# Kernel tuning notes

Measured on AMD Instinct MI355X. Metric: run time of the kernel, lower is better.

## Reference

```python
import jax, jax.numpy as jnp
import numpy as np

NUM_EXPERTS = 4096
NUM_KEYS = 64  # floor(sqrt(num_experts))
TOP_K = 16
NORM_TOPK = False
BN_EPS = 1e-5


def setup_inputs() -> dict:
    key = jax.random.key(0)
    ks = jax.random.split(key, 7)
    B, S, H, I = 2, 2048, 2048, 8192
    s = 0.02
    return {
        "hidden_states": jax.random.normal(ks[0], (B, S, H), jnp.float32),
        "router_gate_w": jax.random.normal(ks[1], (2 * NUM_KEYS, H), jnp.float32) * s,
        "down_embed": jax.random.normal(ks[2], (NUM_EXPERTS, H), jnp.float32) * s,
        "up_embed": jax.random.normal(ks[3], (NUM_EXPERTS, H), jnp.float32) * s,
        "gate_w": jax.random.normal(ks[4], (I, H), jnp.float32) * s,
        "up_w": jax.random.normal(ks[5], (I, H), jnp.float32) * s,
        "down_w": jax.random.normal(ks[6], (H, I), jnp.float32) * s,
    }


def reference(hidden_states, router_gate_w, down_embed, up_embed, gate_w, up_w, down_w):
    B, S, H = hidden_states.shape
    x = hidden_states.reshape(-1, H)  # [N, H]

    # BatchNorm1d(affine=False), training-mode batch statistics (biased var)
    mu = jnp.mean(x, axis=0, keepdims=True)
    var = jnp.mean(jnp.square(x - mu), axis=0, keepdims=True)
    xn = (x - mu) * jax.lax.rsqrt(var + BN_EPS)

    # product-key router: logits [2, N, num_keys]
    rlog = (xn @ router_gate_w.T).reshape(-1, 2, NUM_KEYS).transpose(1, 0, 2)
    logp = jax.nn.log_softmax(rlog, axis=-1)

    # full product scores [N, nk, nk]; top-k over nk*nk candidates
    full = logp[0][:, :, None] + logp[1][:, None, :]
    scores, indices = jax.lax.top_k(full.reshape(-1, NUM_KEYS * NUM_KEYS), TOP_K)
    routing_weights = jnp.exp(scores)  # [N, k]
    if NORM_TOPK:
        routing_weights = routing_weights / jnp.sum(routing_weights, axis=-1, keepdims=True)

    # PEER-style expert: scalar key match then weighted up-embedding sum
    d = down_embed[indices]  # [N, k, H]
    u = up_embed[indices]    # [N, k, H]
    h = jnp.einsum('nh,nkh->nk', x, d)
    experts_states = jnp.einsum('nk,nk,nkh->nh', routing_weights, h, u)

    # dense gated MLP (silu)
    mlp = (jax.nn.silu(x @ gate_w.T) * (x @ up_w.T)) @ down_w.T

    out = (mlp + experts_states).reshape(B, S, H)
    return out, rlog
```

## Files before the change

kernel.cpp:

```cpp
#include <hip/hip_runtime.h>
#include <stdint.h>

#define H_DIM 2048
#define N_TOK 4096
#define I_DIM 8192

typedef __attribute__((ext_vector_type(8))) short short8;
typedef __attribute__((ext_vector_type(4))) float f32x4;

typedef const __attribute__((address_space(1))) unsigned int* gp_t;
typedef __attribute__((address_space(3))) unsigned int* lp_t;

__device__ __forceinline__ void gload16(const unsigned short* g, short* l) {
    __builtin_amdgcn_global_load_lds((gp_t)g, (lp_t)l, 16, 0, 0);
}

__device__ __forceinline__ unsigned short f2bf(float f) {
    union { float f; unsigned int u; } c; c.f = f;
    unsigned int u = c.u;
    return (unsigned short)((u + 0x7FFFu + ((u >> 16) & 1u)) >> 16);
}
__device__ __forceinline__ float bf2f(unsigned short u) {
    union { unsigned int i; float f; } c; c.i = ((unsigned int)u) << 16;
    return c.f;
}

__device__ __forceinline__ float wmax64(float v) {
#pragma unroll
    for (int o = 32; o > 0; o >>= 1) v = fmaxf(v, __shfl_xor(v, o));
    return v;
}
__device__ __forceinline__ float wsum64(float v) {
#pragma unroll
    for (int o = 32; o > 0; o >>= 1) v += __shfl_xor(v, o);
    return v;
}

template<int K, int RSTEP, int LSTEP>
__device__ __forceinline__ void stage4(const unsigned short* src, short* dst) {
#pragma unroll
    for (int j = 0; j < 4; ++j)
        gload16(src + (size_t)j * RSTEP * K, dst + j * LSTEP);
}
template<int K, int RSTEP, int LSTEP>
__device__ __forceinline__ void stage2(const unsigned short* src, short* dst) {
#pragma unroll
    for (int j = 0; j < 2; ++j)
        gload16(src + (size_t)j * RSTEP * K, dst + j * LSTEP);
}

__global__ __launch_bounds__(256) void bn_stats(const float* __restrict__ x,
                                                float* __restrict__ ps, float* __restrict__ pq) {
    int col = blockIdx.x * 256 + threadIdx.x;
    int r0  = blockIdx.y * 128;
    float s = 0.f, q = 0.f;
    for (int r = 0; r < 128; ++r) {
        float v = x[(size_t)(r0 + r) * H_DIM + col];
        s += v; q += v * v;
    }
    ps[blockIdx.y * H_DIM + col] = s;
    pq[blockIdx.y * H_DIM + col] = q;
}

__global__ __launch_bounds__(256) void bn_finalize(const float* __restrict__ ps, const float* __restrict__ pq,
                                                   float* __restrict__ mu, float* __restrict__ rsig) {
    int c = blockIdx.x * 256 + threadIdx.x;
    float s = 0.f, q = 0.f;
    for (int i = 0; i < 32; ++i) { s += ps[i * H_DIM + c]; q += pq[i * H_DIM + c]; }
    float m = s * (1.f / N_TOK);
    float v = q * (1.f / N_TOK) - m * m;
    mu[c] = m;
    rsig[c] = rsqrtf(v + 1e-5f);
}

__global__ __launch_bounds__(256) void cvt_all(const float* __restrict__ gw, const float* __restrict__ uw,
                                               const float* __restrict__ dw, const float* __restrict__ de,
                                               const float* __restrict__ ue, const float* __restrict__ x,
                                               unsigned short* __restrict__ gwb, unsigned short* __restrict__ uwb,
                                               unsigned short* __restrict__ dwb, unsigned short* __restrict__ deb,
                                               unsigned short* __restrict__ ueb, unsigned short* __restrict__ xb) {
    int b = blockIdx.x;
    const float* src; unsigned short* dst; size_t base;
    if      (b < 8192)  { src = gw; dst = gwb; base = (size_t)b; }
    else if (b < 16384) { src = uw; dst = uwb; base = (size_t)(b - 8192); }
    else if (b < 24576) { src = dw; dst = dwb; base = (size_t)(b - 16384); }
    else if (b < 28672) { src = de; dst = deb; base = (size_t)(b - 24576); }
    else if (b < 32768) { src = ue; dst = ueb; base = (size_t)(b - 28672); }
    else                { src = x;  dst = xb;  base = (size_t)(b - 32768); }
    size_t off = (base * 256 + threadIdx.x) * 8;
    float4 a = *(const float4*)(src + off);
    float4 c = *(const float4*)(src + off + 4);
    short8 s;
    s[0]=(short)f2bf(a.x); s[1]=(short)f2bf(a.y); s[2]=(short)f2bf(a.z); s[3]=(short)f2bf(a.w);
    s[4]=(short)f2bf(c.x); s[5]=(short)f2bf(c.y); s[6]=(short)f2bf(c.z); s[7]=(short)f2bf(c.w);
    *(short8*)(dst + off) = s;
}

__global__ __launch_bounds__(256) void cvt_x(const float* __restrict__ x, unsigned short* __restrict__ xb) {
    size_t i = ((size_t)blockIdx.x * 256 + threadIdx.x) * 4;
    float4 v = *(const float4*)(x + i);
    uint2 o;
    o.x = (unsigned)f2bf(v.x) | ((unsigned)f2bf(v.y) << 16);
    o.y = (unsigned)f2bf(v.z) | ((unsigned)f2bf(v.w) << 16);
    *(uint2*)(xb + i) = o;
}

__global__ __launch_bounds__(256) void cvt_w(const float* __restrict__ src, unsigned short* __restrict__ dst) {
    size_t off = ((size_t)blockIdx.x * 256 + threadIdx.x) * 8;
    float4 a = *(const float4*)(src + off);
    float4 b = *(const float4*)(src + off + 4);
    short8 s;
    s[0]=(short)f2bf(a.x); s[1]=(short)f2bf(a.y); s[2]=(short)f2bf(a.z); s[3]=(short)f2bf(a.w);
    s[4]=(short)f2bf(b.x); s[5]=(short)f2bf(b.y); s[6]=(short)f2bf(b.z); s[7]=(short)f2bf(b.w);
    *(short8*)(dst + off) = s;
}

__global__ __launch_bounds__(256) void router_kernel(const float* __restrict__ x, const float* __restrict__ rgw,
                                                     const float* __restrict__ mu, const float* __restrict__ rsig,
                                                     float* __restrict__ rlog) {
    __shared__ float xs[16][65];
    __shared__ float rs[128][65];
    const int t = threadIdx.x;
    const int n0 = blockIdx.x * 16;
    const int tk = t >> 5;
    const int jj = t & 31;
    float acc[2][4] = {{0.f,0.f,0.f,0.f},{0.f,0.f,0.f,0.f}};

    for (int kc = 0; kc < H_DIM; kc += 64) {
        {
            int row = t >> 4, c4 = (t & 15) * 4;
            float4 v = *(const float4*)(x + (size_t)(n0 + row) * H_DIM + kc + c4);
            float4 m = *(const float4*)(mu + kc + c4);
            float4 r = *(const float4*)(rsig + kc + c4);
            xs[row][c4 + 0] = (v.x - m.x) * r.x;
            xs[row][c4 + 1] = (v.y - m.y) * r.y;
            xs[row][c4 + 2] = (v.z - m.z) * r.z;
            xs[row][c4 + 3] = (v.w - m.w) * r.w;
        }
        {
            int row = t >> 1, base = (t & 1) * 32;
            const float* src = rgw + (size_t)row * H_DIM + kc + base;
#pragma unroll
            for (int i = 0; i < 8; ++i) {
                float4 v = *(const float4*)(src + i * 4);
                rs[row][base + i*4 + 0] = v.x;
                rs[row][base + i*4 + 1] = v.y;
                rs[row][base + i*4 + 2] = v.z;
                rs[row][base + i*4 + 3] = v.w;
            }
        }
        __syncthreads();
#pragma unroll 4
        for (int k = 0; k < 64; ++k) {
            float x0 = xs[tk][k], x1 = xs[tk + 8][k];
            float r0 = rs[jj][k], r1 = rs[jj + 32][k], r2 = rs[jj + 64][k], r3 = rs[jj + 96][k];
            acc[0][0] += x0 * r0; acc[0][1] += x0 * r1; acc[0][2] += x0 * r2; acc[0][3] += x0 * r3;
            acc[1][0] += x1 * r0; acc[1][1] += x1 * r1; acc[1][2] += x1 * r2; acc[1][3] += x1 * r3;
        }
        __syncthreads();
    }
#pragma unroll
    for (int a = 0; a < 2; ++a)
#pragma unroll
        for (int b = 0; b < 4; ++b) {
            int n = n0 + tk + 8 * a;
            int j = jj + 32 * b;
            rlog[(size_t)(j >> 6) * (N_TOK * 64) + (size_t)n * 64 + (j & 63)] = acc[a][b];
        }
}

__global__ __launch_bounds__(256) void topk_kernel(const float* __restrict__ rlog,
                                                   float* __restrict__ topw, int* __restrict__ topi) {
    const int lane = threadIdx.x & 63;
    const int n = blockIdx.x * 4 + (threadIdx.x >> 6);

    float a = rlog[(size_t)n * 64 + lane];
    float b = rlog[(size_t)(N_TOK * 64) + (size_t)n * 64 + lane];
    float ma = wmax64(a);
    float lpa = a - ma - logf(wsum64(expf(a - ma)));
    float mb = wmax64(b);
    float lpb = b - mb - logf(wsum64(expf(b - mb)));

    float va = lpa, vb = lpb;
    float tva = -1e30f, tvb = -1e30f; int tia = 0, tib = 0;
    for (int it = 0; it < 16; ++it) {
        float mx = wmax64(va);
        int w = __ffsll(__ballot(va == mx)) - 1;
        if (lane == it) { tva = mx; tia = w; }
        if (lane == w) va = -1e30f;
        mx = wmax64(vb);
        w = __ffsll(__ballot(vb == mx)) - 1;
        if (lane == it) { tvb = mx; tib = w; }
        if (lane == w) vb = -1e30f;
    }
    float av = __shfl(tva, lane >> 2);
    int   ai = __shfl(tia, lane >> 2);
    int   q0 = (lane & 3) * 4;
    float c0 = av + __shfl(tvb, q0 + 0); int b0 = __shfl(tib, q0 + 0);
    float c1 = av + __shfl(tvb, q0 + 1); int b1 = __shfl(tib, q0 + 1);
    float c2 = av + __shfl(tvb, q0 + 2); int b2 = __shfl(tib, q0 + 2);
    float c3 = av + __shfl(tvb, q0 + 3); int b3 = __shfl(tib, q0 + 3);

    for (int it = 0; it < 16; ++it) {
        float lv = c0; int lq = 0;
        if (c1 > lv) { lv = c1; lq = 1; }
        if (c2 > lv) { lv = c2; lq = 2; }
        if (c3 > lv) { lv = c3; lq = 3; }
        float mx = wmax64(lv);
        int w = __ffsll(__ballot(lv == mx)) - 1;
        if (lane == w) {
            int bj;
            switch (lq) {
                case 0:  bj = b0; c0 = -1e30f; break;
                case 1:  bj = b1; c1 = -1e30f; break;
                case 2:  bj = b2; c2 = -1e30f; break;
                default: bj = b3; c3 = -1e30f; break;
            }
            topw[n * 16 + it] = expf(mx);
            topi[n * 16 + it] = ai * 64 + bj;
        }
    }
}

__global__ __launch_bounds__(256) void experts_kernel_b(const float* __restrict__ x, const unsigned short* __restrict__ de,
                                                        const unsigned short* __restrict__ ue, const float* __restrict__ topw,
                                                        const int* __restrict__ topi, float* __restrict__ out) {
    __shared__ float psum[16][4];
    const int n = blockIdx.x;
    const int t = threadIdx.x, lane = t & 63, wid = t >> 6;

    float xr[8];
    {
        float4 v0 = *(const float4*)(x + (size_t)n * H_DIM + t * 8);
        float4 v1 = *(const float4*)(x + (size_t)n * H_DIM + t * 8 + 4);
        xr[0]=v0.x; xr[1]=v0.y; xr[2]=v0.z; xr[3]=v0.w;
        xr[4]=v1.x; xr[5]=v1.y; xr[6]=v1.z; xr[7]=v1.w;
    }
    int   eidx[16];
    float ew[16];
#pragma unroll
    for (int k = 0; k < 16; ++k) { eidx[k] = topi[n * 16 + k]; ew[k] = topw[n * 16 + k]; }

#pragma unroll
    for (int k = 0; k < 16; ++k) {
        short8 d = *(const short8*)(de + (size_t)eidx[k] * H_DIM + t * 8);
        float p = 0.f;
#pragma unroll
        for (int j = 0; j < 8; ++j) p += bf2f((unsigned short)d[j]) * xr[j];
        p = wsum64(p);
        if (lane == 0) psum[k][wid] = p;
    }
    __syncthreads();

    float acc[8] = {0,0,0,0,0,0,0,0};
#pragma unroll
    for (int k = 0; k < 16; ++k) {
        float h = psum[k][0] + psum[k][1] + psum[k][2] + psum[k][3];
        float coef = ew[k] * h;
        short8 u = *(const short8*)(ue + (size_t)eidx[k] * H_DIM + t * 8);
#pragma unroll
        for (int j = 0; j < 8; ++j) acc[j] += coef * bf2f((unsigned short)u[j]);
    }
    float4 o0 = {acc[0], acc[1], acc[2], acc[3]};
    float4 o1 = {acc[4], acc[5], acc[6], acc[7]};
    *(float4*)(out + (size_t)n * H_DIM + t * 8)     = o0;
    *(float4*)(out + (size_t)n * H_DIM + t * 8 + 4) = o1;
}

__global__ __launch_bounds__(256) void experts_kernel(const float* __restrict__ x, const float* __restrict__ de,
                                                      const float* __restrict__ ue, const float* __restrict__ topw,
                                                      const int* __restrict__ topi, float* __restrict__ out) {
    __shared__ float psum[16][4];
    const int n = blockIdx.x;
    const int t = threadIdx.x, lane = t & 63, wid = t >> 6;

    float xr[8];
    {
        float4 v0 = *(const float4*)(x + (size_t)n * H_DIM + t * 8);
        float4 v1 = *(const float4*)(x + (size_t)n * H_DIM + t * 8 + 4);
        xr[0]=v0.x; xr[1]=v0.y; xr[2]=v0.z; xr[3]=v0.w;
        xr[4]=v1.x; xr[5]=v1.y; xr[6]=v1.z; xr[7]=v1.w;
    }
    int   eidx[16];
    float ew[16];
#pragma unroll
    for (int k = 0; k < 16; ++k) { eidx[k] = topi[n * 16 + k]; ew[k] = topw[n * 16 + k]; }

#pragma unroll
    for (int k = 0; k < 16; ++k) {
        const float* dr = de + (size_t)eidx[k] * H_DIM + t * 8;
        float4 v0 = *(const float4*)dr;
        float4 v1 = *(const float4*)(dr + 4);
        float p = v0.x*xr[0] + v0.y*xr[1] + v0.z*xr[2] + v0.w*xr[3]
                + v1.x*xr[4] + v1.y*xr[5] + v1.z*xr[6] + v1.w*xr[7];
        p = wsum64(p);
        if (lane == 0) psum[k][wid] = p;
    }
    __syncthreads();

    float acc[8] = {0,0,0,0,0,0,0,0};
#pragma unroll
    for (int k = 0; k < 16; ++k) {
        float h = psum[k][0] + psum[k][1] + psum[k][2] + psum[k][3];
        float coef = ew[k] * h;
        const float* ur = ue + (size_t)eidx[k] * H_DIM + t * 8;
        float4 v0 = *(const float4*)ur;
        float4 v1 = *(const float4*)(ur + 4);
        acc[0] += coef * v0.x; acc[1] += coef * v0.y; acc[2] += coef * v0.z; acc[3] += coef * v0.w;
        acc[4] += coef * v1.x; acc[5] += coef * v1.y; acc[6] += coef * v1.z; acc[7] += coef * v1.w;
    }
    float4 o0 = {acc[0], acc[1], acc[2], acc[3]};
    float4 o1 = {acc[4], acc[5], acc[6], acc[7]};
    *(float4*)(out + (size_t)n * H_DIM + t * 8)     = o0;
    *(float4*)(out + (size_t)n * H_DIM + t * 8 + 4) = o1;
}

#define SWZB(row, byteoff) ((byteoff) ^ (((row) & 7) << 4))

#define NTGU (H_DIM / 64)

__global__ __launch_bounds__(512, 2) void gemm_gu256(const unsigned short* __restrict__ xb,
                                                     const unsigned short* __restrict__ gwb,
                                                     const unsigned short* __restrict__ uwb,
                                                     unsigned short* __restrict__ act) {
    __shared__ __attribute__((aligned(16))) short sA[2][16384];
    __shared__ __attribute__((aligned(16))) short sBg[2][8192];
    __shared__ __attribute__((aligned(16))) short sBu[2][8192];
    const int t = threadIdx.x;
    const int lane = t & 63, wid = t >> 6;
    const int wm = wid >> 1, wn = wid & 1;
    const int l15 = lane & 15, l4 = lane >> 4;
    const int bid = blockIdx.x;
    const int sw = (bid & 7) * 128 + (bid >> 3);
    const int bx = sw & 63, by = sw >> 6;
    const int row0 = by * 256, col0 = bx * 128;

    const int rseg = lane >> 3;
    const int chunk = (lane & 7) ^ rseg;
    const unsigned short* aSrc = xb  + (size_t)(row0 + wid * 8 + rseg) * H_DIM + chunk * 8;
    const unsigned short* gSrc = gwb + (size_t)(col0 + wid * 8 + rseg) * H_DIM + chunk * 8;
    const unsigned short* uSrc = uwb + (size_t)(col0 + wid * 8 + rseg) * H_DIM + chunk * 8;

    const int swzb = (l15 & 7) << 4;
    const int kx0 = (l4 * 16) ^ swzb;
    const int kx1 = (64 + l4 * 16) ^ swzb;
    const int arow = (wm * 64 + l15) * 64;
    const int brow = (wn * 64 + l15) * 64;

    f32x4 zero = {0.f, 0.f, 0.f, 0.f};
    f32x4 accg[4][4], accu[4][4];
#pragma unroll
    for (int m = 0; m < 4; ++m)
#pragma unroll
        for (int n = 0; n < 4; ++n) { accg[m][n] = zero; accu[m][n] = zero; }

    stage4<H_DIM, 64, 4096>(aSrc, &sA[0][wid * 512]);
    stage2<H_DIM, 64, 4096>(gSrc, &sBg[0][wid * 512]);
    stage2<H_DIM, 64, 4096>(uSrc, &sBu[0][wid * 512]);
    __syncthreads();

    int cur = 0;
    for (int g = 0; g < NTGU; ++g) {
        if (g + 1 < NTGU) {
            stage4<H_DIM, 64, 4096>(aSrc + (size_t)(g + 1) * 64, &sA[cur ^ 1][wid * 512]);
            stage2<H_DIM, 64, 4096>(gSrc + (size_t)(g + 1) * 64, &sBg[cur ^ 1][wid * 512]);
            stage2<H_DIM, 64, 4096>(uSrc + (size_t)(g + 1) * 64, &sBu[cur ^ 1][wid * 512]);
        }
        const short* Ac = &sA[cur][0];
        const short* Gc = &sBg[cur][0];
        const short* Uc = &sBu[cur][0];
        {
            short8 a0[4], bg0[4], bu0[4];
#pragma unroll
            for (int m = 0; m < 4; ++m) a0[m]  = *(const short8*)(Ac + arow + m * 1024 + (kx0 >> 1));
#pragma unroll
            for (int n = 0; n < 4; ++n) bg0[n] = *(const short8*)(Gc + brow + n * 1024 + (kx0 >> 1));
#pragma unroll
            for (int n = 0; n < 4; ++n) bu0[n] = *(const short8*)(Uc + brow + n * 1024 + (kx0 >> 1));
            __builtin_amdgcn_s_setprio(1);
#pragma unroll
            for (int m = 0; m < 4; ++m)
#pragma unroll
                for (int n = 0; n < 4; ++n) {
                    accg[m][n] = __builtin_amdgcn_mfma_f32_16x16x32_bf16(a0[m], bg0[n], accg[m][n], 0, 0, 0);
                    accu[m][n] = __builtin_amdgcn_mfma_f32_16x16x32_bf16(a0[m], bu0[n], accu[m][n], 0, 0, 0);
                }
            __builtin_amdgcn_s_setprio(0);
        }
        {
            short8 a1[4], bg1[4], bu1[4];
#pragma unroll
            for (int m = 0; m < 4; ++m) a1[m]  = *(const short8*)(Ac + arow + m * 1024 + (kx1 >> 1));
#pragma unroll
            for (int n = 0; n < 4; ++n) bg1[n] = *(const short8*)(Gc + brow + n * 1024 + (kx1 >> 1));
#pragma unroll
            for (int n = 0; n < 4; ++n) bu1[n] = *(const short8*)(Uc + brow + n * 1024 + (kx1 >> 1));
            __builtin_amdgcn_s_setprio(1);
#pragma unroll
            for (int m = 0; m < 4; ++m)
#pragma unroll
                for (int n = 0; n < 4; ++n) {
                    accg[m][n] = __builtin_amdgcn_mfma_f32_16x16x32_bf16(a1[m], bg1[n], accg[m][n], 0, 0, 0);
                    accu[m][n] = __builtin_amdgcn_mfma_f32_16x16x32_bf16(a1[m], bu1[n], accu[m][n], 0, 0, 0);
                }
            __builtin_amdgcn_s_setprio(0);
        }
        __syncthreads();
        cur ^= 1;
    }

    const int rbase = row0 + wm * 64, cbase = col0 + wn * 64;
#pragma unroll
    for (int m = 0; m < 4; ++m)
#pragma unroll
        for (int n = 0; n < 4; ++n)
#pragma unroll
            for (int j = 0; j < 4; ++j) {
                int r = rbase + m * 16 + l4 * 4 + j;
                int c2 = cbase + n * 16 + l15;
                float gv = accg[m][n][j];
                float uv = accu[m][n][j];
                float sv = gv / (1.f + expf(-gv));
                act[(size_t)r * I_DIM + c2] = f2bf(sv * uv);
            }
}

#define NTD (I_DIM / 64)

__global__ __launch_bounds__(256, 2) void gemm_down128(const unsigned short* __restrict__ act,
                                                       const unsigned short* __restrict__ dwb,
                                                       float* __restrict__ out) {
    __shared__ __attribute__((aligned(16))) short sA[2][8192];
    __shared__ __attribute__((aligned(16))) short sB[2][8192];
    const int t = threadIdx.x;
    const int lane = t & 63, wid = t >> 6;
    const int wm = wid >> 1, wn = wid & 1;
    const int l15 = lane & 15, l4 = lane >> 4;
    const int bid = blockIdx.x;
    const int sw = (bid & 7) * 64 + (bid >> 3);
    const int bx = sw & 15, by = sw >> 4;
    const int row0 = by * 128, col0 = bx * 128;

    const int rseg = lane >> 3;
    const int chunk = (lane & 7) ^ rseg;
    const unsigned short* aSrc = act + (size_t)(row0 + wid * 8 + rseg) * I_DIM + chunk * 8;
    const unsigned short* bSrc = dwb + (size_t)(col0 + wid * 8 + rseg) * I_DIM + chunk * 8;

    const int swzb = (l15 & 7) << 4;
    const int kx0 = (l4 * 16) ^ swzb;
    const int kx1 = (64 + l4 * 16) ^ swzb;
    const int arow = (wm * 64 + l15) * 64;
    const int brow = (wn * 64 + l15) * 64;

    f32x4 zero = {0.f, 0.f, 0.f, 0.f};
    f32x4 acc[4][4];
#pragma unroll
    for (int m = 0; m < 4; ++m)
#pragma unroll
        for (int n = 0; n < 4; ++n) acc[m][n] = zero;

    stage4<I_DIM, 32, 2048>(aSrc, &sA[0][wid * 512]);
    stage4<I_DIM, 32, 2048>(bSrc, &sB[0][wid * 512]);
    __syncthreads();

    int cur = 0;
    for (int g = 0; g < NTD; ++g) {
        if (g + 1 < NTD) {
            stage4<I_DIM, 32, 2048>(aSrc + (size_t)(g + 1) * 64, &sA[cur ^ 1][wid * 512]);
            stage4<I_DIM, 32, 2048>(bSrc + (size_t)(g + 1) * 64, &sB[cur ^ 1][wid * 512]);
        }
        const short* Ac = &sA[cur][0];
        const short* Bc = &sB[cur][0];
        {
            short8 a0[4], b0[4];
#pragma unroll
            for (int m = 0; m < 4; ++m) a0[m] = *(const short8*)(Ac + arow + m * 1024 + (kx0 >> 1));
#pragma unroll
            for (int n = 0; n < 4; ++n) b0[n] = *(const short8*)(Bc + brow + n * 1024 + (kx0 >> 1));
            __builtin_amdgcn_s_setprio(1);
#pragma unroll
            for (int m = 0; m < 4; ++m)
#pragma unroll
                for (int n = 0; n < 4; ++n)
                    acc[m][n] = __builtin_amdgcn_mfma_f32_16x16x32_bf16(a0[m], b0[n], acc[m][n], 0, 0, 0);
            __builtin_amdgcn_s_setprio(0);
        }
        {
            short8 a1[4], b1[4];
#pragma unroll
            for (int m = 0; m < 4; ++m) a1[m] = *(const short8*)(Ac + arow + m * 1024 + (kx1 >> 1));
#pragma unroll
            for (int n = 0; n < 4; ++n) b1[n] = *(const short8*)(Bc + brow + n * 1024 + (kx1 >> 1));
            __builtin_amdgcn_s_setprio(1);
#pragma unroll
            for (int m = 0; m < 4; ++m)
#pragma unroll
                for (int n = 0; n < 4; ++n)
                    acc[m][n] = __builtin_amdgcn_mfma_f32_16x16x32_bf16(a1[m], b1[n], acc[m][n], 0, 0, 0);
            __builtin_amdgcn_s_setprio(0);
        }
        __syncthreads();
        cur ^= 1;
    }

    const int rbase = row0 + wm * 64, cbase = col0 + wn * 64;
#pragma unroll
    for (int m = 0; m < 4; ++m)
#pragma unroll
        for (int n = 0; n < 4; ++n)
#pragma unroll
            for (int j = 0; j < 4; ++j) {
                int r = rbase + m * 16 + l4 * 4 + j;
                int c2 = cbase + n * 16 + l15;
                out[(size_t)r * H_DIM + c2] += acc[m][n][j];
            }
}

__global__ __launch_bounds__(256) void gemm_gu(const unsigned short* __restrict__ xb,
                                               const float* __restrict__ gw, const float* __restrict__ uw,
                                               unsigned short* __restrict__ act) {
    __shared__ __attribute__((aligned(16))) short As[128 * 64];
    __shared__ __attribute__((aligned(16))) short Bg[128 * 64];
    __shared__ __attribute__((aligned(16))) short Bu[128 * 64];
    const int t = threadIdx.x;
    const int lane = t & 63, wid = t >> 6;
    const int wr = wid >> 1, wc = wid & 1;
    const int l15 = lane & 15, l4 = lane >> 4;
    const int row0 = blockIdx.y * 128;
    const int col0 = blockIdx.x * 128;
    const int srow = t >> 1, shalf = (t & 1) * 32;

    f32x4 zero = {0.f, 0.f, 0.f, 0.f};
    f32x4 accg[4][4], accu[4][4];
#pragma unroll
    for (int m = 0; m < 4; ++m)
#pragma unroll
        for (int n = 0; n < 4; ++n) { accg[m][n] = zero; accu[m][n] = zero; }

    for (int kt = 0; kt < H_DIM; kt += 64) {
        {
            const unsigned short* src = xb + (size_t)(row0 + srow) * H_DIM + kt + shalf;
#pragma unroll
            for (int i = 0; i < 4; ++i) {
                int boff = SWZB(srow, (shalf + i * 8) * 2);
                *(short8*)(As + srow * 64 + (boff >> 1)) = *(const short8*)(src + i * 8);
            }
        }
        {
            const float* g = gw + (size_t)(col0 + srow) * H_DIM + kt + shalf;
            const float* u = uw + (size_t)(col0 + srow) * H_DIM + kt + shalf;
#pragma unroll
            for (int i = 0; i < 4; ++i) {
                int boff = SWZB(srow, (shalf + i * 8) * 2);
                float4 a0 = *(const float4*)(g + i * 8);
                float4 a1 = *(const float4*)(g + i * 8 + 4);
                short8 s;
                s[0]=(short)f2bf(a0.x); s[1]=(short)f2bf(a0.y); s[2]=(short)f2bf(a0.z); s[3]=(short)f2bf(a0.w);
                s[4]=(short)f2bf(a1.x); s[5]=(short)f2bf(a1.y); s[6]=(short)f2bf(a1.z); s[7]=(short)f2bf(a1.w);
                *(short8*)(Bg + srow * 64 + (boff >> 1)) = s;
                float4 b0 = *(const float4*)(u + i * 8);
                float4 b1 = *(const float4*)(u + i * 8 + 4);
                short8 r;
                r[0]=(short)f2bf(b0.x); r[1]=(short)f2bf(b0.y); r[2]=(short)f2bf(b0.z); r[3]=(short)f2bf(b0.w);
                r[4]=(short)f2bf(b1.x); r[5]=(short)f2bf(b1.y); r[6]=(short)f2bf(b1.z); r[7]=(short)f2bf(b1.w);
                *(short8*)(Bu + srow * 64 + (boff >> 1)) = r;
            }
        }
        __syncthreads();
#pragma unroll
        for (int kk = 0; kk < 64; kk += 32) {
            short8 af[4], bgf[4], buf_[4];
#pragma unroll
            for (int m = 0; m < 4; ++m) {
                int row = wr * 64 + m * 16 + l15;
                af[m] = *(const short8*)(As + row * 64 + (SWZB(row, (kk + l4 * 8) * 2) >> 1));
            }
#pragma unroll
            for (int n = 0; n < 4; ++n) {
                int row = wc * 64 + n * 16 + l15;
                int off = row * 64 + (SWZB(row, (kk + l4 * 8) * 2) >> 1);
                bgf[n]  = *(const short8*)(Bg + off);
                buf_[n] = *(const short8*)(Bu + off);
            }
#pragma unroll
            for (int m = 0; m < 4; ++m)
#pragma unroll
                for (int n = 0; n < 4; ++n) {
                    accg[m][n] = __builtin_amdgcn_mfma_f32_16x16x32_bf16(af[m], bgf[n],  accg[m][n], 0, 0, 0);
                    accu[m][n] = __builtin_amdgcn_mfma_f32_16x16x32_bf16(af[m], buf_[n], accu[m][n], 0, 0, 0);
                }
        }
        __syncthreads();
    }
    const int rbase = row0 + wr * 64, cbase = col0 + wc * 64;
#pragma unroll
    for (int m = 0; m < 4; ++m)
#pragma unroll
        for (int n = 0; n < 4; ++n)
#pragma unroll
            for (int j = 0; j < 4; ++j) {
                int r = rbase + m * 16 + l4 * 4 + j;
                int c = cbase + n * 16 + l15;
                float gv = accg[m][n][j];
                float uv = accu[m][n][j];
                float sv = gv / (1.f + expf(-gv));
                act[(size_t)r * I_DIM + c] = f2bf(sv * uv);
            }
}

__global__ __launch_bounds__(256) void gemm_down(const unsigned short* __restrict__ act,
                                                 const float* __restrict__ dw, float* __restrict__ out) {
    __shared__ __attribute__((aligned(16))) short As[128 * 64];
    __shared__ __attribute__((aligned(16))) short Bs[128 * 64];
    const int t = threadIdx.x;
    const int lane = t & 63, wid = t >> 6;
    const int wr = wid >> 1, wc = wid & 1;
    const int l15 = lane & 15, l4 = lane >> 4;
    const int row0 = blockIdx.y * 128;
    const int col0 = blockIdx.x * 128;
    const int srow = t >> 1, shalf = (t & 1) * 32;

    f32x4 zero = {0.f, 0.f, 0.f, 0.f};
    f32x4 acc[4][4];
#pragma unroll
    for (int m = 0; m < 4; ++m)
#pragma unroll
        for (int n = 0; n < 4; ++n) acc[m][n] = zero;

    for (int kt = 0; kt < I_DIM; kt += 64) {
        {
            const unsigned short* src = act + (size_t)(row0 + srow) * I_DIM + kt + shalf;
#pragma unroll
            for (int i = 0; i < 4; ++i) {
                int boff = SWZB(srow, (shalf + i * 8) * 2);
                *(short8*)(As + srow * 64 + (boff >> 1)) = *(const short8*)(src + i * 8);
            }
        }
        {
            const float* g = dw + (size_t)(col0 + srow) * I_DIM + kt + shalf;
#pragma unroll
            for (int i = 0; i < 4; ++i) {
                int boff = SWZB(srow, (shalf + i * 8) * 2);
                float4 a0 = *(const float4*)(g + i * 8);
                float4 a1 = *(const float4*)(g + i * 8 + 4);
                short8 s;
                s[0]=(short)f2bf(a0.x); s[1]=(short)f2bf(a0.y); s[2]=(short)f2bf(a0.z); s[3]=(short)f2bf(a0.w);
                s[4]=(short)f2bf(a1.x); s[5]=(short)f2bf(a1.y); s[6]=(short)f2bf(a1.z); s[7]=(short)f2bf(a1.w);
                *(short8*)(Bs + srow * 64 + (boff >> 1)) = s;
            }
        }
        __syncthreads();
#pragma unroll
        for (int kk = 0; kk < 64; kk += 32) {
            short8 af[4], bf[4];
#pragma unroll
            for (int m = 0; m < 4; ++m) {
                int row = wr * 64 + m * 16 + l15;
                af[m] = *(const short8*)(As + row * 64 + (SWZB(row, (kk + l4 * 8) * 2) >> 1));
            }
#pragma unroll
            for (int n = 0; n < 4; ++n) {
                int row = wc * 64 + n * 16 + l15;
                bf[n] = *(const short8*)(Bs + row * 64 + (SWZB(row, (kk + l4 * 8) * 2) >> 1));
            }
#pragma unroll
            for (int m = 0; m < 4; ++m)
#pragma unroll
                for (int n = 0; n < 4; ++n)
                    acc[m][n] = __builtin_amdgcn_mfma_f32_16x16x32_bf16(af[m], bf[n], acc[m][n], 0, 0, 0);
        }
        __syncthreads();
    }
    const int rbase = row0 + wr * 64, cbase = col0 + wc * 64;
#pragma unroll
    for (int m = 0; m < 4; ++m)
#pragma unroll
        for (int n = 0; n < 4; ++n)
#pragma unroll
            for (int j = 0; j < 4; ++j) {
                int r = rbase + m * 16 + l4 * 4 + j;
                int c = cbase + n * 16 + l15;
                out[(size_t)r * H_DIM + c] += acc[m][n][j];
            }
}

extern "C" void kernel_launch(void* const* d_in, const int* in_sizes, int n_in,
                              void* d_out, int out_size, void* d_ws, size_t ws_size,
                              hipStream_t stream) {
    const float* x   = (const float*)d_in[0];
    const float* rgw = (const float*)d_in[1];
    const float* de  = (const float*)d_in[2];
    const float* ue  = (const float*)d_in[3];
    const float* gw  = (const float*)d_in[4];
    const float* uw  = (const float*)d_in[5];
    const float* dw  = (const float*)d_in[6];
    float* out = (float*)d_out;
    char* ws = (char*)d_ws;

    float* ps   = (float*)(ws + 0);
    float* pq   = (float*)(ws + 262144);
    float* mu   = (float*)(ws + 524288);
    float* rsig = (float*)(ws + 532480);
    float* topw = (float*)(ws + 540672);
    int*   topi = (int*)  (ws + 802816);
    unsigned short* xb  = (unsigned short*)(ws + 1179648);
    unsigned short* act = (unsigned short*)(ws + 17956864);
    unsigned short* gwb = (unsigned short*)(ws + 85065728);
    unsigned short* uwb = (unsigned short*)(ws + 118620160);
    unsigned short* dwb = (unsigned short*)(ws + 152174592);
    unsigned short* deb = (unsigned short*)(ws + 185729024);
    unsigned short* ueb = (unsigned short*)(ws + 202506240);
    float* rlog = out + 8388608;
    const bool fast  = ws_size >= 185729024ULL;
    const bool fast2 = ws_size >= 219283456ULL;

    bn_stats   <<<dim3(8, 32), 256, 0, stream>>>(x, ps, pq);
    bn_finalize<<<8, 256, 0, stream>>>(ps, pq, mu, rsig);
    router_kernel<<<256, 256, 0, stream>>>(x, rgw, mu, rsig, rlog);
    topk_kernel<<<1024, 256, 0, stream>>>(rlog, topw, topi);

    if (fast2) {
        cvt_all<<<36864, 256, 0, stream>>>(gw, uw, dw, de, ue, x, gwb, uwb, dwb, deb, ueb, xb);
        experts_kernel_b<<<4096, 256, 0, stream>>>(x, deb, ueb, topw, topi, out);
        gemm_gu256<<<1024, 512, 0, stream>>>(xb, gwb, uwb, act);
        gemm_down128<<<512, 256, 0, stream>>>(act, dwb, out);
    } else if (fast) {
        cvt_x<<<8192, 256, 0, stream>>>(x, xb);
        cvt_w<<<8192, 256, 0, stream>>>(gw, gwb);
        cvt_w<<<8192, 256, 0, stream>>>(uw, uwb);
        cvt_w<<<8192, 256, 0, stream>>>(dw, dwb);
        experts_kernel<<<4096, 256, 0, stream>>>(x, de, ue, topw, topi, out);
        gemm_gu256<<<1024, 512, 0, stream>>>(xb, gwb, uwb, act);
        gemm_down128<<<512, 256, 0, stream>>>(act, dwb, out);
    } else {
        cvt_x<<<8192, 256, 0, stream>>>(x, xb);
        experts_kernel<<<4096, 256, 0, stream>>>(x, de, ue, topw, topi, out);
        gemm_gu  <<<dim3(64, 32), 256, 0, stream>>>(xb, gw, uw, act);
        gemm_down<<<dim3(16, 32), 256, 0, stream>>>(act, dw, out);
    }
}
```

Baseline: 756.1 us.

## Enlarge down-projection GEMM tile to 256x128 with triple-buffered LDS pipeline

The down-projection GEMM moves from a 128x128 tile with 256 threads to a 256x128 tile with 512 threads, halving the grid to 256 blocks. The LDS ring grows from double to triple buffering, with loads issued two stages ahead. The full __syncthreads is replaced by an explicit vmcnt wait plus s_barrier so global-to-LDS loads stay in flight across iterations. The aim is better operand reuse and more overlap of memory latency, at the cost of more LDS per block, fewer blocks than CUs, and a hand-tuned wait count that must match the number of issued loads.

```diff
diff --git a/kernel.cpp b/kernel.cpp
--- a/kernel.cpp
+++ b/kernel.cpp
@@ -427,19 +427,19 @@
 
 #define NTD (I_DIM / 64)
 
-__global__ __launch_bounds__(256, 2) void gemm_down128(const unsigned short* __restrict__ act,
-                                                       const unsigned short* __restrict__ dwb,
-                                                       float* __restrict__ out) {
-    __shared__ __attribute__((aligned(16))) short sA[2][8192];
-    __shared__ __attribute__((aligned(16))) short sB[2][8192];
+__global__ __launch_bounds__(512) void gemm_down256(const unsigned short* __restrict__ act,
+                                                    const unsigned short* __restrict__ dwb,
+                                                    float* __restrict__ out) {
+    __shared__ __attribute__((aligned(16))) short sA[3][16384];
+    __shared__ __attribute__((aligned(16))) short sB[3][8192];
     const int t = threadIdx.x;
     const int lane = t & 63, wid = t >> 6;
-    const int wm = wid >> 1, wn = wid & 1;
+    const int wm = wid >> 2, wn = wid & 3;
     const int l15 = lane & 15, l4 = lane >> 4;
     const int bid = blockIdx.x;
-    const int sw = (bid & 7) * 64 + (bid >> 3);
+    const int sw = (bid & 7) * 32 + (bid >> 3);
     const int bx = sw & 15, by = sw >> 4;
-    const int row0 = by * 128, col0 = bx * 128;
+    const int row0 = by * 256, col0 = bx * 128;
 
     const int rseg = lane >> 3;
     const int chunk = (lane & 7) ^ rseg;
@@ -449,65 +449,77 @@
     const int swzb = (l15 & 7) << 4;
     const int kx0 = (l4 * 16) ^ swzb;
     const int kx1 = (64 + l4 * 16) ^ swzb;
-    const int arow = (wm * 64 + l15) * 64;
-    const int brow = (wn * 64 + l15) * 64;
+    const int arow = (wm * 128 + l15) * 64;
+    const int brow0 = (wn * 32 + l15) * 64;
 
     f32x4 zero = {0.f, 0.f, 0.f, 0.f};
-    f32x4 acc[4][4];
-#pragma unroll
-    for (int m = 0; m < 4; ++m)
-#pragma unroll
-        for (int n = 0; n < 4; ++n) acc[m][n] = zero;
-
-    stage4<I_DIM, 32, 2048>(aSrc, &sA[0][wid * 512]);
-    stage4<I_DIM, 32, 2048>(bSrc, &sB[0][wid * 512]);
-    __syncthreads();
-
-    int cur = 0;
+    f32x4 acc[8][2];
+#pragma unroll
+    for (int m = 0; m < 8; ++m)
+#pragma unroll
+        for (int n = 0; n < 2; ++n) acc[m][n] = zero;
+
+    stage4<I_DIM, 64, 4096>(aSrc,      &sA[0][wid * 512]);
+    stage2<I_DIM, 64, 4096>(bSrc,      &sB[0][wid * 512]);
+    stage4<I_DIM, 64, 4096>(aSrc + 64, &sA[1][wid * 512]);
+    stage2<I_DIM, 64, 4096>(bSrc + 64, &sB[1][wid * 512]);
+    __builtin_amdgcn_sched_barrier(0);
+    asm volatile("s_waitcnt vmcnt(6)" ::: "memory");
+    __builtin_amdgcn_sched_barrier(0);
+    __builtin_amdgcn_s_barrier();
+    asm volatile("" ::: "memory");
+
     for (int g = 0; g < NTD; ++g) {
-        if (g + 1 < NTD) {
-            stage4<I_DIM, 32, 2048>(aSrc + (size_t)(g + 1) * 64, &sA[cur ^ 1][wid * 512]);
-            stage4<I_DIM, 32, 2048>(bSrc + (size_t)(g + 1) * 64, &sB[cur ^ 1][wid * 512]);
-        }
-        const short* Ac = &sA[cur][0];
-        const short* Bc = &sB[cur][0];
-        {
-            short8 a0[4], b0[4];
-#pragma unroll
-            for (int m = 0; m < 4; ++m) a0[m] = *(const short8*)(Ac + arow + m * 1024 + (kx0 >> 1));
-#pragma unroll
-            for (int n = 0; n < 4; ++n) b0[n] = *(const short8*)(Bc + brow + n * 1024 + (kx0 >> 1));
+        const int cb = g % 3;
+        if (g + 2 < NTD) {
+            const int nb = (g + 2) % 3;
+            stage4<I_DIM, 64, 4096>(aSrc + (size_t)(g + 2) * 64, &sA[nb][wid * 512]);
+            stage2<I_DIM, 64, 4096>(bSrc + (size_t)(g + 2) * 64, &sB[nb][wid * 512]);
+        }
+        __builtin_amdgcn_sched_barrier(0);
+        const short* Ac = &sA[cb][0];
+        const short* Bc = &sB[cb][0];
+        {
+            short8 a0[8], b0[2];
+#pragma unroll
+            for (int m = 0; m < 8; ++m) a0[m] = *(const short8*)(Ac + arow + m * 1024 + (kx0 >> 1));
+#pragma unroll
+            for (int n = 0; n < 2; ++n) b0[n] = *(const short8*)(Bc + brow0 + n * 1024 + (kx0 >> 1));
             __builtin_amdgcn_s_setprio(1);
 #pragma unroll
-            for (int m = 0; m < 4; ++m)
-#pragma unroll
-                for (int n = 0; n < 4; ++n)
+            for (int m = 0; m < 8; ++m)
+#pragma unroll
+                for (int n = 0; n < 2; ++n)
                     acc[m][n] = __builtin_amdgcn_mfma_f32_16x16x32_bf16(a0[m], b0[n], acc[m][n], 0, 0, 0);
             __builtin_amdgcn_s_setprio(0);
         }
         {
-            short8 a1[4], b1[4];
-#pragma unroll
-            for (int m = 0; m < 4; ++m) a1[m] = *(const short8*)(Ac + arow + m * 1024 + (kx1 >> 1));
-#pragma unroll
-            for (int n = 0; n < 4; ++n) b1[n] = *(const short8*)(Bc + brow + n * 1024 + (kx1 >> 1));
+            short8 a1[8], b1[2];
+#pragma unroll
+            for (int m = 0; m < 8; ++m) a1[m] = *(const short8*)(Ac + arow + m * 1024 + (kx1 >> 1));
+#pragma unroll
+            for (int n = 0; n < 2; ++n) b1[n] = *(const short8*)(Bc + brow0 + n * 1024 + (kx1 >> 1));
             __builtin_amdgcn_s_setprio(1);
 #pragma unroll
-            for (int m = 0; m < 4; ++m)
-#pragma unroll
-                for (int n = 0; n < 4; ++n)
+            for (int m = 0; m < 8; ++m)
+#pragma unroll
+                for (int n = 0; n < 2; ++n)
                     acc[m][n] = __builtin_amdgcn_mfma_f32_16x16x32_bf16(a1[m], b1[n], acc[m][n], 0, 0, 0);
             __builtin_amdgcn_s_setprio(0);
         }
-        __syncthreads();
-        cur ^= 1;
-    }
-
-    const int rbase = row0 + wm * 64, cbase = col0 + wn * 64;
-#pragma unroll
-    for (int m = 0; m < 4; ++m)
-#pragma unroll
-        for (int n = 0; n < 4; ++n)
+        __builtin_amdgcn_sched_barrier(0);
+        if (g + 2 < NTD) { asm volatile("s_waitcnt vmcnt(6)" ::: "memory"); }
+        else             { asm volatile("s_waitcnt vmcnt(0)" ::: "memory"); }
+        __builtin_amdgcn_sched_barrier(0);
+        __builtin_amdgcn_s_barrier();
+        asm volatile("" ::: "memory");
+    }
+
+    const int rbase = row0 + wm * 128, cbase = col0 + wn * 32;
+#pragma unroll
+    for (int m = 0; m < 8; ++m)
+#pragma unroll
+        for (int n = 0; n < 2; ++n)
 #pragma unroll
             for (int j = 0; j < 4; ++j) {
                 int r = rbase + m * 16 + l4 * 4 + j;
@@ -723,7 +735,7 @@
         cvt_all<<<36864, 256, 0, stream>>>(gw, uw, dw, de, ue, x, gwb, uwb, dwb, deb, ueb, xb);
         experts_kernel_b<<<4096, 256, 0, stream>>>(x, deb, ueb, topw, topi, out);
         gemm_gu256<<<1024, 512, 0, stream>>>(xb, gwb, uwb, act);
-        gemm_down128<<<512, 256, 0, stream>>>(act, dwb, out);
+        gemm_down256<<<256, 512, 0, stream>>>(act, dwb, out);
     } else if (fast) {
         cvt_x<<<8192, 256, 0, stream>>>(x, xb);
         cvt_w<<<8192, 256, 0, stream>>>(gw, gwb);
@@ -731,7 +743,7 @@
         cvt_w<<<8192, 256, 0, stream>>>(dw, dwb);
         experts_kernel<<<4096, 256, 0, stream>>>(x, de, ue, topw, topi, out);
         gemm_gu256<<<1024, 512, 0, stream>>>(xb, gwb, uwb, act);
-        gemm_down128<<<512, 256, 0, stream>>>(act, dwb, out);
+        gemm_down256<<<256, 512, 0, stream>>>(act, dwb, out);
     } else {
         cvt_x<<<8192, 256, 0, stream>>>(x, xb);
         experts_kernel<<<4096, 256, 0, stream>>>(x, de, ue, topw, topi, out);
```

Result: slower. 806.1 us (+6.6%).
